# Kernel optimization log

Measured on AMD Instinct MI355X. Metric: run time of the kernel, lower is better.

Reference implementation:

```python
import jax, jax.numpy as jnp
import numpy as np

EPS = 1e-3  # layer epsilon
B, T, D, K = 16, 2048, 256, 8


def setup_inputs() -> dict:
    key = jax.random.key(0)
    k1, k2, k3, k4 = jax.random.split(key, 4)
    x = jax.random.normal(k1, (B, T, D), dtype=jnp.float32)
    # custom_mean_initializer: U(-1, 1)
    mean = jax.random.uniform(k2, (K, D), minval=-1.0, maxval=1.0, dtype=jnp.float32)
    # custom_variance_initializer: U(0.001, 0.01)
    variance = jax.random.uniform(k3, (K, D), minval=0.001, maxval=0.01, dtype=jnp.float32)
    # custom_prior_initializer: U(0.01, 0.99), normalized over cluster axis
    p0 = jax.random.uniform(k4, (K, 1), minval=0.01, maxval=0.99, dtype=jnp.float32)
    prior = p0 / jnp.sum(p0, axis=0)
    return {"x": x, "mean": mean, "variance": variance, "prior": prior}


def _ucb_norm(x, mean, variance, prior):
    eps = EPS
    var = jax.nn.softplus(variance)                      # (K,D)
    # NB: TF applies softmax over the last axis of (K,1) -> all ones; reproduced faithfully.
    pri = jax.nn.softmax(prior, axis=-1)[:, 0]           # (K,)
    d = x[None] - mean[:, None, None, :]                 # (K,B,T,D)
    # per-feature unnormalized responsibilities (elementwise, as in the TF code)
    p = pri[:, None, None, None] * jnp.exp(-0.5 * d * d / (var[:, None, None, :] + eps))
    tau = p / (jnp.sum(p, axis=0, keepdims=True) + eps)  # (K,B,T,D)
    # sum over batch + middle axes -> (K,1,1,D)
    hat_tau = tau / (jnp.sum(tau, axis=(1, 2), keepdims=True) + eps)
    prod = hat_tau * x[None]                             # (K,B,T,D)
    expectation = jnp.mean(prod, axis=2, keepdims=True)  # (K,B,1,D)
    v = x[None] - expectation
    var_k = jnp.mean(hat_tau * prod * prod, axis=2, keepdims=True)  # (K,B,1,D)
    hat_x_k = v / jnp.sqrt(var_k + eps)
    scale = tau / jnp.sqrt(pri + eps)[:, None, None, None]
    return jnp.sum(scale * hat_x_k, axis=0)              # (B,T,D)


def reference(x, mean, variance, prior):
    return _ucb_norm(x, mean, variance, prior)
```

## Files before the change

### kernel.cpp

```cpp
#include <hip/hip_runtime.h>

#define EPS 1e-3f
#define Bn 16
#define Tn 2048
#define Dn 256
#define Kn 8
#define TS2 128
#define TCH2 (Tn / TS2)

#define KBD ((size_t)Kn * Bn * Dn)
#define KD  ((size_t)Kn * Dn)

__device__ __forceinline__ float fexp2(float x) {
#if __has_builtin(__builtin_amdgcn_exp2f)
    return __builtin_amdgcn_exp2f(x);
#else
    return exp2f(x);
#endif
}

__device__ __forceinline__ float frcp(float x) {
#if __has_builtin(__builtin_amdgcn_rcpf)
    return __builtin_amdgcn_rcpf(x);
#else
    return 1.0f / x;
#endif
}

__global__ __launch_bounds__(256) void ucb_coef(
    const float* __restrict__ Mean, const float* __restrict__ Var,
    float* __restrict__ CA, float* __restrict__ CB, float* __restrict__ CG)
{
    int i = blockIdx.x * 256 + threadIdx.x;
    const float L2E = 1.4426950408889634f;
    float m  = Mean[i];
    float v  = Var[i];
    float sp = logf(1.0f + expf(v));
    float c2 = -0.5f * L2E / (sp + EPS);
    CA[i] = c2;
    CB[i] = -2.0f * c2 * m;
    CG[i] = c2 * m * m;
}

__global__ __launch_bounds__(256) void ucb_pass1(
    const float* __restrict__ X,
    const float* __restrict__ CA, const float* __restrict__ CB,
    const float* __restrict__ CG,
    float* __restrict__ P0, float* __restrict__ P1, float* __restrict__ P3,
    int tch)
{
    const int d  = threadIdx.x;
    const int tc = blockIdx.x;
    const int b  = blockIdx.y;

    float Ak[Kn], Bk[Kn], Gk[Kn];
#pragma unroll
    for (int k = 0; k < Kn; ++k) {
        Ak[k] = CA[k * Dn + d];
        Bk[k] = CB[k * Dn + d];
        Gk[k] = CG[k * Dn + d];
    }

    float s0[Kn], s1[Kn], s3[Kn];
#pragma unroll
    for (int k = 0; k < Kn; ++k) { s0[k] = 0.f; s1[k] = 0.f; s3[k] = 0.f; }

    const float* xp = X + ((size_t)b * Tn + (size_t)tc * tch) * Dn + d;
#pragma unroll 4
    for (int t = 0; t < tch; ++t) {
        float x = xp[(size_t)t * Dn];
        float p[Kn];
        float sum = EPS;
#pragma unroll
        for (int k = 0; k < Kn; ++k) {
            float arg = fmaf(fmaf(Ak[k], x, Bk[k]), x, Gk[k]);
            p[k] = fexp2(arg);
            sum += p[k];
        }
        float inv = frcp(sum);
        float xx  = x * x;
#pragma unroll
        for (int k = 0; k < Kn; ++k) {
            float tau = p[k] * inv;
            s0[k] += tau;
            s1[k]  = fmaf(tau, x, s1[k]);
            float t3 = tau * tau * tau;
            s3[k]  = fmaf(t3, xx, s3[k]);
        }
    }

#pragma unroll
    for (int k = 0; k < Kn; ++k) {
        size_t o = (size_t)tc * KBD + ((size_t)(k * Bn + b) << 8) + d;
        P0[o] = s0[k];
        P1[o] = s1[k];
        P3[o] = s3[k];
    }
}

__global__ __launch_bounds__(256) void ucb_reduce(
    const float* __restrict__ P0, const float* __restrict__ P1,
    const float* __restrict__ P3,
    float* __restrict__ S0, float* __restrict__ A1, float* __restrict__ A3,
    int ts1)
{
    size_t idx = (size_t)blockIdx.x * 256 + threadIdx.x;
    float a = 0.f, b = 0.f, c = 0.f;
#pragma unroll 4
    for (int tc = 0; tc < ts1; ++tc) {
        size_t o = (size_t)tc * KBD + idx;
        a += P0[o];
        b += P1[o];
        c += P3[o];
    }
    S0[idx] = a;
    A1[idx] = b;
    A3[idx] = c;
}

__global__ __launch_bounds__(256) void ucb_mid(
    const float* __restrict__ S0, const float* __restrict__ A1,
    const float* __restrict__ A3,
    float* __restrict__ R, float* __restrict__ RE)
{
    int idx = blockIdx.x * 256 + threadIdx.x;
    int k = idx >> 12;
    int d = idx & (Dn - 1);

    float s = EPS;
#pragma unroll
    for (int b2 = 0; b2 < Bn; ++b2)
        s += S0[((size_t)k * Bn + b2) * Dn + d];
    float iS = 1.0f / s;

    const float rs = rsqrtf(1.0f + EPS);
    float a1 = A1[idx];
    float a3 = A3[idx];
    float E  = a1 * iS * (1.0f / Tn);
    float V  = a3 * iS * iS * iS * (1.0f / Tn);
    float r  = rs * rsqrtf(V + EPS);
    R[idx]  = r;
    RE[idx] = r * E;
}

__global__ __launch_bounds__(256) void ucb_pass2(
    const float* __restrict__ X,
    const float* __restrict__ CA, const float* __restrict__ CB,
    const float* __restrict__ CG,
    const float* __restrict__ R, const float* __restrict__ RE,
    float* __restrict__ Out)
{
    const int d  = threadIdx.x;
    const int tc = blockIdx.x;
    const int b  = blockIdx.y;

    float Ak[Kn], Bk[Kn], Gk[Kn], Rk[Kn], REk[Kn];
#pragma unroll
    for (int k = 0; k < Kn; ++k) {
        Ak[k] = CA[k * Dn + d];
        Bk[k] = CB[k * Dn + d];
        Gk[k] = CG[k * Dn + d];
        size_t idx = ((size_t)k * Bn + b) * Dn + d;
        Rk[k]  = R[idx];
        REk[k] = RE[idx];
    }

    const size_t base = ((size_t)b * Tn + (size_t)tc * TCH2) * Dn + d;
#pragma unroll 4
    for (int t = 0; t < TCH2; ++t) {
        float x = X[base + (size_t)t * Dn];
        float p[Kn];
        float sum = EPS;
#pragma unroll
        for (int k = 0; k < Kn; ++k) {
            float arg = fmaf(fmaf(Ak[k], x, Bk[k]), x, Gk[k]);
            p[k] = fexp2(arg);
            sum += p[k];
        }
        float inv = frcp(sum);
        float acc = 0.f;
#pragma unroll
        for (int k = 0; k < Kn; ++k) {
            acc = fmaf(p[k], fmaf(Rk[k], x, -REk[k]), acc);
        }
        Out[base + (size_t)t * Dn] = acc * inv;
    }
}

extern "C" void kernel_launch(void* const* d_in, const int* in_sizes, int n_in,
                              void* d_out, int out_size, void* d_ws, size_t ws_size,
                              hipStream_t stream)
{
    const float* x    = (const float*)d_in[0];
    const float* mean = (const float*)d_in[1];
    const float* var  = (const float*)d_in[2];

    int ts1 = 64;
    while (ts1 > 4) {
        size_t need = (3 * (size_t)ts1 * KBD + 5 * KBD + 3 * KD) * sizeof(float);
        if (need <= ws_size) break;
        ts1 >>= 1;
    }
    const int tch1 = Tn / ts1;

    float* P0 = (float*)d_ws;
    float* P1 = P0 + (size_t)ts1 * KBD;
    float* P3 = P1 + (size_t)ts1 * KBD;
    float* S0 = P3 + (size_t)ts1 * KBD;
    float* A1 = S0 + KBD;
    float* A3 = A1 + KBD;
    float* R  = A3 + KBD;
    float* RE = R  + KBD;
    float* CA = RE + KBD;
    float* CB = CA + KD;
    float* CG = CB + KD;

    ucb_coef<<<dim3(KD / 256), dim3(256), 0, stream>>>(mean, var, CA, CB, CG);

    ucb_pass1<<<dim3(ts1, Bn), dim3(256), 0, stream>>>(x, CA, CB, CG, P0, P1, P3, tch1);

    ucb_reduce<<<dim3(KBD / 256), dim3(256), 0, stream>>>(P0, P1, P3, S0, A1, A3, ts1);

    ucb_mid<<<dim3(KBD / 256), dim3(256), 0, stream>>>(S0, A1, A3, R, RE);

    ucb_pass2<<<dim3(TS2, Bn), dim3(256), 0, stream>>>(x, CA, CB, CG, R, RE, (float*)d_out);
}
```

Baseline: 60.10 us.

## Fold coef kernel into passes, split partial reduction across groups, simplify tau math

Drops the separate coefficient kernel and recomputes softplus-derived coefficients per thread inside pass1 and pass2, removing one launch. The partial-sum reduction is split over three arrays and four groups, giving 12x more blocks, and ucb_mid finishes the last group sum. The pass1 inner loop multiplies by precomputed q, xq and x²q³ instead of forming tau per cluster, saving multiplies. The cost is some redundant transcendental work per thread and slightly more workspace traffic in mid.

```diff
diff --git a/kernel.cpp b/kernel.cpp
--- a/kernel.cpp
+++ b/kernel.cpp
@@ -9,7 +9,7 @@
 #define TCH2 (Tn / TS2)
 
 #define KBD ((size_t)Kn * Bn * Dn)
-#define KD  ((size_t)Kn * Dn)
+#define NG  4
 
 __device__ __forceinline__ float fexp2(float x) {
 #if __has_builtin(__builtin_amdgcn_exp2f)
@@ -27,25 +27,26 @@
 #endif
 }
 
-__global__ __launch_bounds__(256) void ucb_coef(
-    const float* __restrict__ Mean, const float* __restrict__ Var,
-    float* __restrict__ CA, float* __restrict__ CB, float* __restrict__ CG)
-{
-    int i = blockIdx.x * 256 + threadIdx.x;
+__device__ __forceinline__ void load_coefs(
+    const float* __restrict__ Mean, const float* __restrict__ Var, int d,
+    float* Ak, float* Bk, float* Gk)
+{
     const float L2E = 1.4426950408889634f;
-    float m  = Mean[i];
-    float v  = Var[i];
-    float sp = logf(1.0f + expf(v));
-    float c2 = -0.5f * L2E / (sp + EPS);
-    CA[i] = c2;
-    CB[i] = -2.0f * c2 * m;
-    CG[i] = c2 * m * m;
+#pragma unroll
+    for (int k = 0; k < Kn; ++k) {
+        float m  = Mean[k * Dn + d];
+        float v  = Var[k * Dn + d];
+        float sp = logf(1.0f + expf(v));
+        float c2 = -0.5f * L2E / (sp + EPS);
+        Ak[k] = c2;
+        Bk[k] = -2.0f * c2 * m;
+        Gk[k] = c2 * m * m;
+    }
 }
 
 __global__ __launch_bounds__(256) void ucb_pass1(
     const float* __restrict__ X,
-    const float* __restrict__ CA, const float* __restrict__ CB,
-    const float* __restrict__ CG,
+    const float* __restrict__ Mean, const float* __restrict__ Var,
     float* __restrict__ P0, float* __restrict__ P1, float* __restrict__ P3,
     int tch)
 {
@@ -54,12 +55,7 @@
     const int b  = blockIdx.y;
 
     float Ak[Kn], Bk[Kn], Gk[Kn];
-#pragma unroll
-    for (int k = 0; k < Kn; ++k) {
-        Ak[k] = CA[k * Dn + d];
-        Bk[k] = CB[k * Dn + d];
-        Gk[k] = CG[k * Dn + d];
-    }
+    load_coefs(Mean, Var, d, Ak, Bk, Gk);
 
     float s0[Kn], s1[Kn], s3[Kn];
 #pragma unroll
@@ -77,15 +73,18 @@
             p[k] = fexp2(arg);
             sum += p[k];
         }
-        float inv = frcp(sum);
-        float xx  = x * x;
-#pragma unroll
-        for (int k = 0; k < Kn; ++k) {
-            float tau = p[k] * inv;
-            s0[k] += tau;
-            s1[k]  = fmaf(tau, x, s1[k]);
-            float t3 = tau * tau * tau;
-            s3[k]  = fmaf(t3, xx, s3[k]);
+        float q    = frcp(sum);
+        float xq   = x * q;
+        float q2   = q * q;
+        float xxq3 = (x * x) * (q2 * q);
+#pragma unroll
+        for (int k = 0; k < Kn; ++k) {
+            float pk = p[k];
+            float p2 = pk * pk;
+            float p3 = p2 * pk;
+            s0[k] = fmaf(pk, q,    s0[k]);
+            s1[k] = fmaf(pk, xq,   s1[k]);
+            s3[k] = fmaf(p3, xxq3, s3[k]);
         }
     }
 
@@ -98,44 +97,48 @@
     }
 }
 
-__global__ __launch_bounds__(256) void ucb_reduce(
-    const float* __restrict__ P0, const float* __restrict__ P1,
-    const float* __restrict__ P3,
-    float* __restrict__ S0, float* __restrict__ A1, float* __restrict__ A3,
-    int ts1)
-{
-    size_t idx = (size_t)blockIdx.x * 256 + threadIdx.x;
-    float a = 0.f, b = 0.f, c = 0.f;
+__global__ __launch_bounds__(256) void ucb_reduceA(
+    const float* __restrict__ P, float* __restrict__ Q, int ts1)
+{
+    const size_t idx = (size_t)blockIdx.x * 256 + threadIdx.x;
+    const int arr = blockIdx.y;
+    const int g   = blockIdx.z;
+    const int per = ts1 / NG;
+
+    const float* p = P + ((size_t)arr * ts1 + (size_t)g * per) * KBD + idx;
+    float a = 0.f;
 #pragma unroll 4
-    for (int tc = 0; tc < ts1; ++tc) {
-        size_t o = (size_t)tc * KBD + idx;
-        a += P0[o];
-        b += P1[o];
-        c += P3[o];
-    }
-    S0[idx] = a;
-    A1[idx] = b;
-    A3[idx] = c;
+    for (int i = 0; i < per; ++i)
+        a += p[(size_t)i * KBD];
+    Q[((size_t)(arr * NG + g)) * KBD + idx] = a;
 }
 
 __global__ __launch_bounds__(256) void ucb_mid(
-    const float* __restrict__ S0, const float* __restrict__ A1,
-    const float* __restrict__ A3,
+    const float* __restrict__ Q,
     float* __restrict__ R, float* __restrict__ RE)
 {
-    int idx = blockIdx.x * 256 + threadIdx.x;
-    int k = idx >> 12;
-    int d = idx & (Dn - 1);
+    const size_t idx = (size_t)blockIdx.x * 256 + threadIdx.x;
+    const int k = (int)(idx >> 12);
+    const int d = (int)(idx & (Dn - 1));
 
     float s = EPS;
 #pragma unroll
-    for (int b2 = 0; b2 < Bn; ++b2)
-        s += S0[((size_t)k * Bn + b2) * Dn + d];
-    float iS = 1.0f / s;
+    for (int g = 0; g < NG; ++g) {
+        const float* q0 = Q + (size_t)g * KBD + ((size_t)k << 12) + d;
+#pragma unroll
+        for (int b2 = 0; b2 < Bn; ++b2)
+            s += q0[(size_t)b2 << 8];
+    }
+    float iS = frcp(s);
+
+    float a1 = 0.f, a3 = 0.f;
+#pragma unroll
+    for (int g = 0; g < NG; ++g) {
+        a1 += Q[((size_t)(NG + g))     * KBD + idx];
+        a3 += Q[((size_t)(2 * NG + g)) * KBD + idx];
+    }
 
     const float rs = rsqrtf(1.0f + EPS);
-    float a1 = A1[idx];
-    float a3 = A3[idx];
     float E  = a1 * iS * (1.0f / Tn);
     float V  = a3 * iS * iS * iS * (1.0f / Tn);
     float r  = rs * rsqrtf(V + EPS);
@@ -145,8 +148,7 @@
 
 __global__ __launch_bounds__(256) void ucb_pass2(
     const float* __restrict__ X,
-    const float* __restrict__ CA, const float* __restrict__ CB,
-    const float* __restrict__ CG,
+    const float* __restrict__ Mean, const float* __restrict__ Var,
     const float* __restrict__ R, const float* __restrict__ RE,
     float* __restrict__ Out)
 {
@@ -154,12 +156,12 @@
     const int tc = blockIdx.x;
     const int b  = blockIdx.y;
 
-    float Ak[Kn], Bk[Kn], Gk[Kn], Rk[Kn], REk[Kn];
+    float Ak[Kn], Bk[Kn], Gk[Kn];
+    load_coefs(Mean, Var, d, Ak, Bk, Gk);
+
+    float Rk[Kn], REk[Kn];
 #pragma unroll
     for (int k = 0; k < Kn; ++k) {
-        Ak[k] = CA[k * Dn + d];
-        Bk[k] = CB[k * Dn + d];
-        Gk[k] = CG[k * Dn + d];
         size_t idx = ((size_t)k * Bn + b) * Dn + d;
         Rk[k]  = R[idx];
         REk[k] = RE[idx];
@@ -196,8 +198,8 @@
     const float* var  = (const float*)d_in[2];
 
     int ts1 = 64;
-    while (ts1 > 4) {
-        size_t need = (3 * (size_t)ts1 * KBD + 5 * KBD + 3 * KD) * sizeof(float);
+    while (ts1 > NG) {
+        size_t need = (3 * (size_t)ts1 * KBD + 3 * NG * KBD + 2 * KBD) * sizeof(float);
         if (need <= ws_size) break;
         ts1 >>= 1;
     }
@@ -206,22 +208,15 @@
     float* P0 = (float*)d_ws;
     float* P1 = P0 + (size_t)ts1 * KBD;
     float* P3 = P1 + (size_t)ts1 * KBD;
-    float* S0 = P3 + (size_t)ts1 * KBD;
-    float* A1 = S0 + KBD;
-    float* A3 = A1 + KBD;
-    float* R  = A3 + KBD;
+    float* Q  = P3 + (size_t)ts1 * KBD;
+    float* R  = Q  + 3 * NG * KBD;
     float* RE = R  + KBD;
-    float* CA = RE + KBD;
-    float* CB = CA + KD;
-    float* CG = CB + KD;
-
-    ucb_coef<<<dim3(KD / 256), dim3(256), 0, stream>>>(mean, var, CA, CB, CG);
-
-    ucb_pass1<<<dim3(ts1, Bn), dim3(256), 0, stream>>>(x, CA, CB, CG, P0, P1, P3, tch1);
-
-    ucb_reduce<<<dim3(KBD / 256), dim3(256), 0, stream>>>(P0, P1, P3, S0, A1, A3, ts1);
-
-    ucb_mid<<<dim3(KBD / 256), dim3(256), 0, stream>>>(S0, A1, A3, R, RE);
-
-    ucb_pass2<<<dim3(TS2, Bn), dim3(256), 0, stream>>>(x, CA, CB, CG, R, RE, (float*)d_out);
-}
+
+    ucb_pass1<<<dim3(ts1, Bn), dim3(256), 0, stream>>>(x, mean, var, P0, P1, P3, tch1);
+
+    ucb_reduceA<<<dim3(KBD / 256, 3, NG), dim3(256), 0, stream>>>(P0, Q, ts1);
+
+    ucb_mid<<<dim3(KBD / 256), dim3(256), 0, stream>>>(Q, R, RE);
+
+    ucb_pass2<<<dim3(TS2, Bn), dim3(256), 0, stream>>>(x, mean, var, R, RE, (float*)d_out);
+}
```

Measured after the change: 59.23 us. No clear change (-1.4%).
